# Kernel tuning notes

Measured on AMD Instinct MI355X. Metric: run time of the kernel, lower is better.

Reference implementation:

```python
import jax, jax.numpy as jnp
import numpy as np

NUM_GRAPHS = 100  # batch of graphs for pooling (dgl.max_nodes / WeightAndSum)


def _glorot(k, shape):
    lim = np.sqrt(6.0 / (shape[0] + shape[1])).astype(np.float32)
    return jax.random.uniform(k, shape, jnp.float32, -lim, lim)


def setup_inputs() -> dict:
    key = jax.random.key(0)
    ks = jax.random.split(key, 10)
    N, E, D, H = 100000, 1600000, 128, 128
    node_feats = jax.random.normal(ks[0], (N, D), dtype=jnp.float32)
    src = jax.random.randint(ks[1], (E,), 0, N, dtype=jnp.int32)
    dst = jax.random.randint(ks[2], (E,), 0, N, dtype=jnp.int32)
    graph_ids = jnp.sort(jax.random.randint(ks[3], (N,), 0, NUM_GRAPHS, dtype=jnp.int32))
    W1 = _glorot(ks[4], (D, H)); b1 = jnp.zeros((H,), jnp.float32)
    W2 = _glorot(ks[5], (H, H)); b2 = jnp.zeros((H,), jnp.float32)
    W3 = _glorot(ks[6], (H, H)); b3 = jnp.zeros((H,), jnp.float32)
    W_pool = _glorot(ks[7], (H, 1)); b_pool = jnp.zeros((1,), jnp.float32)
    return {"node_feats": node_feats, "src": src, "dst": dst, "graph_ids": graph_ids,
            "W1": W1, "b1": b1, "W2": W2, "b2": b2, "W3": W3, "b3": b3,
            "W_pool": W_pool, "b_pool": b_pool}


def _gcn_layer(h, W, b, src, dst, norm_src, norm_dst, N):
    # DGL GraphConv, norm='both': D_dst^{-1/2} (A^T (D_src^{-1/2} X W)) + b
    h = (h * norm_src[:, None]) @ W                      # [N, H]
    agg = jax.ops.segment_sum(h[src], dst, num_segments=N)  # gather + scatter-add
    return agg * norm_dst[:, None] + b


def reference(node_feats, src, dst, graph_ids, W1, b1, W2, b2, W3, b3, W_pool, b_pool):
    N = node_feats.shape[0]
    # dgl.add_self_loop (allow_zero_in_degree=False)
    loops = jnp.arange(N, dtype=src.dtype)
    src_sl = jnp.concatenate([src, loops])
    dst_sl = jnp.concatenate([dst, loops])
    ones = jnp.ones(src_sl.shape, jnp.float32)
    out_deg = jax.ops.segment_sum(ones, src_sl, num_segments=N)
    in_deg = jax.ops.segment_sum(ones, dst_sl, num_segments=N)
    norm_src = jax.lax.rsqrt(jnp.maximum(out_deg, 1.0))
    norm_dst = jax.lax.rsqrt(jnp.maximum(in_deg, 1.0))
    h = node_feats
    for W, b in ((W1, b1), (W2, b2), (W3, b3)):
        h = jax.nn.relu(_gcn_layer(h, W, b, src_sl, dst_sl, norm_src, norm_dst, N))
    # pooling_func: WeightAndSum (sigmoid-gated weighted sum per graph) + max_nodes
    w = jax.nn.sigmoid(h @ W_pool + b_pool)              # [N, 1]
    g_sum = jax.ops.segment_sum(h * w, graph_ids, num_segments=NUM_GRAPHS)
    g_max = jax.ops.segment_max(h, graph_ids, num_segments=NUM_GRAPHS)
    return jnp.concatenate([g_sum, g_max], axis=1)       # [G, 2H]
```

## Files before the change

kernel.cpp:

```cpp
#include <hip/hip_runtime.h>
#include <hip/hip_bf16.h>

#define DIM 128
#define CAP 64

typedef __attribute__((ext_vector_type(8))) short bf16x8;
typedef __attribute__((ext_vector_type(4))) float f32x4;
union U16 { uint4 u; bf16x8 b; };

__device__ __forceinline__ unsigned short f2bf(float f) {
    unsigned u = __float_as_uint(f);
    unsigned r = (u + 0x7fffu + ((u >> 16) & 1u)) >> 16;
    return (unsigned short)r;
}
__device__ __forceinline__ unsigned pack2bf(float a, float b) {
    return (unsigned)f2bf(a) | ((unsigned)f2bf(b) << 16);
}
__device__ __forceinline__ float2 unpack2bf(unsigned v) {
    float2 r;
    r.x = __uint_as_float(v << 16);
    r.y = __uint_as_float(v & 0xffff0000u);
    return r;
}
__device__ __forceinline__ void accum8(float* acc, uint4 v) {
    float2 f0 = unpack2bf(v.x), f1 = unpack2bf(v.y);
    float2 f2 = unpack2bf(v.z), f3 = unpack2bf(v.w);
    acc[0] += f0.x; acc[1] += f0.y; acc[2] += f1.x; acc[3] += f1.y;
    acc[4] += f2.x; acc[5] += f2.y; acc[6] += f3.x; acc[7] += f3.y;
}

__global__ __launch_bounds__(256) void k_build_gemm(const int* __restrict__ src,
                                                    const int* __restrict__ dst,
                                                    int* __restrict__ in_cnt,
                                                    int* __restrict__ out_cnt,
                                                    int* __restrict__ csr_pad, int E,
                                                    const float* __restrict__ x,
                                                    const float* __restrict__ W,
                                                    unsigned* __restrict__ xwb, int N,
                                                    int buildGrid, int mmGrid) {
    if (blockIdx.x & 1) {
        int bid = blockIdx.x >> 1;
        if (bid >= buildGrid) return;
        int e0 = (bid * 256 + threadIdx.x) * 4;
        int s[4], d[4], pos[4];
#pragma unroll
        for (int i = 0; i < 4; i++) {
            int e = e0 + i;
            if (e < E) { s[i] = src[e]; d[i] = dst[e]; }
        }
#pragma unroll
        for (int i = 0; i < 4; i++) {
            if (e0 + i < E) atomicAdd(&out_cnt[s[i]], 1);
        }
#pragma unroll
        for (int i = 0; i < 4; i++) {
            if (e0 + i < E) pos[i] = atomicAdd(&in_cnt[d[i]], 1);
        }
#pragma unroll
        for (int i = 0; i < 4; i++) {
            if (e0 + i < E && pos[i] < CAP) csr_pad[d[i] * CAP + pos[i]] = s[i];
        }
        return;
    }
    int bid = blockIdx.x >> 1;
    if (bid >= mmGrid) return;
    __shared__ float sW[32][128];
    __shared__ float sX[32][64];
    int t = threadIdx.x;
    int ty = t >> 4;
    int tx = t & 15;
    int nodeBase = bid * 64;

    float acc[4][8];
#pragma unroll
    for (int m = 0; m < 4; m++)
#pragma unroll
        for (int j = 0; j < 8; j++) acc[m][j] = 0.f;

    int ln = t & 63;
    int kb = (t >> 6) * 8;
    int nd = nodeBase + ln;

#pragma unroll 1
    for (int kc = 0; kc < DIM; kc += 32) {
#pragma unroll
        for (int i = 0; i < 4; i++) {
            int v = t + i * 256;
            int kk = v >> 5;
            int cc = (v & 31) * 4;
            *(float4*)&sW[kk][cc] = *(const float4*)&W[(kc + kk) * DIM + cc];
        }
        float4 a0, a1;
        if (nd < N) {
            a0 = *(const float4*)&x[nd * DIM + kc + kb];
            a1 = *(const float4*)&x[nd * DIM + kc + kb + 4];
        } else {
            a0 = make_float4(0, 0, 0, 0);
            a1 = make_float4(0, 0, 0, 0);
        }
        sX[kb + 0][ln] = a0.x;
        sX[kb + 1][ln] = a0.y;
        sX[kb + 2][ln] = a0.z;
        sX[kb + 3][ln] = a0.w;
        sX[kb + 4][ln] = a1.x;
        sX[kb + 5][ln] = a1.y;
        sX[kb + 6][ln] = a1.z;
        sX[kb + 7][ln] = a1.w;
        __syncthreads();

#pragma unroll
        for (int k = 0; k < 32; k++) {
            float4 xv = *(float4*)&sX[k][ty * 4];
            float4 wa = *(float4*)&sW[k][tx * 4];
            float4 wb = *(float4*)&sW[k][tx * 4 + 64];
            float xm[4] = {xv.x, xv.y, xv.z, xv.w};
#pragma unroll
            for (int m = 0; m < 4; m++) {
                acc[m][0] += xm[m] * wa.x;
                acc[m][1] += xm[m] * wa.y;
                acc[m][2] += xm[m] * wa.z;
                acc[m][3] += xm[m] * wa.w;
                acc[m][4] += xm[m] * wb.x;
                acc[m][5] += xm[m] * wb.y;
                acc[m][6] += xm[m] * wb.z;
                acc[m][7] += xm[m] * wb.w;
            }
        }
        __syncthreads();
    }

#pragma unroll
    for (int m = 0; m < 4; m++) {
        int n2 = nodeBase + ty * 4 + m;
        if (n2 < N) {
            uint2 q0, q1;
            q0.x = pack2bf(acc[m][0], acc[m][1]);
            q0.y = pack2bf(acc[m][2], acc[m][3]);
            q1.x = pack2bf(acc[m][4], acc[m][5]);
            q1.y = pack2bf(acc[m][6], acc[m][7]);
            *(uint2*)&xwb[n2 * 64 + tx * 2] = q0;
            *(uint2*)&xwb[n2 * 64 + 32 + tx * 2] = q1;
        }
    }
}

__global__ void k_finish(const int* __restrict__ in_cnt, const int* __restrict__ out_cnt,
                         float* __restrict__ nsrc, float* __restrict__ ndst, int N) {
    int i = blockIdx.x * blockDim.x + threadIdx.x;
    if (i < N) {
        nsrc[i] = rsqrtf((float)(out_cnt[i] + 1));
        ndst[i] = rsqrtf((float)(in_cnt[i] + 1));
    }
}

__global__ __launch_bounds__(256) void k_scale(unsigned* __restrict__ xwb,
                                               const float* __restrict__ nsrc, int total) {
    int i = blockIdx.x * blockDim.x + threadIdx.x;
    if (i < total) {
        float s = nsrc[i >> 6];
        float2 v = unpack2bf(xwb[i]);
        xwb[i] = pack2bf(v.x * s, v.y * s);
    }
}

__global__ __launch_bounds__(256) void k_xw_mfma(const unsigned* __restrict__ hb,
                                                 const float* __restrict__ nsrc,
                                                 const float* __restrict__ W,
                                                 unsigned* __restrict__ xwb, int N) {
    __shared__ unsigned wT[128 * 68];
    int t = threadIdx.x;
    {
        int n = t >> 1;
        int kp0 = (t & 1) * 32;
#pragma unroll
        for (int i = 0; i < 32; i++) {
            int kp = kp0 + i;
            wT[n * 68 + kp] = pack2bf(W[(2 * kp) * DIM + n], W[(2 * kp + 1) * DIM + n]);
        }
    }
    __syncthreads();
    int wave = t >> 6, lane = t & 63;
    int quad = lane >> 4, c = lane & 15;
    int m = blockIdx.x * 64 + wave * 16 + c;
    bool mv = m < N;
    f32x4 acc[8];
#pragma unroll
    for (int i = 0; i < 8; i++) acc[i] = (f32x4){0.f, 0.f, 0.f, 0.f};

#pragma unroll
    for (int ks = 0; ks < 4; ks++) {
        U16 av;
        if (mv) av.u = *(const uint4*)&hb[m * 64 + ks * 16 + quad * 4];
        else av.u = make_uint4(0, 0, 0, 0);
#pragma unroll
        for (int cb = 0; cb < 8; cb++) {
            U16 bv;
            bv.u = *(const uint4*)&wT[(cb * 16 + c) * 68 + ks * 16 + quad * 4];
            acc[cb] = __builtin_amdgcn_mfma_f32_16x16x32_bf16(av.b, bv.b, acc[cb], 0, 0, 0);
        }
    }
    int rowBase = blockIdx.x * 64 + wave * 16 + quad * 4;
#pragma unroll
    for (int r = 0; r < 4; r++) {
        int rowN = rowBase + r;
        float nrm = (rowN < N) ? nsrc[rowN] : 0.f;
#pragma unroll
        for (int cb = 0; cb < 8; cb++) {
            float v = acc[cb][r] * nrm;
            float vn = __shfl_xor(v, 1, 64);
            if (((c & 1) == 0) && rowN < N)
                xwb[rowN * 64 + cb * 8 + (c >> 1)] = pack2bf(v, vn);
        }
    }
}

template <bool GATED>
__device__ __forceinline__ void agg_body(const uint4* __restrict__ xwb4,
                                         const int* __restrict__ in_cnt,
                                         const int* __restrict__ csr_pad,
                                         const float* __restrict__ ndst,
                                         const float* __restrict__ bias,
                                         uint4* __restrict__ hb4,
                                         const float* __restrict__ Wp,
                                         const float* __restrict__ bp,
                                         float* __restrict__ wg, int N) {
    int gid = blockIdx.x * blockDim.x + threadIdx.x;
    int n = gid >> 6;
    int lane = gid & 63;
    if (n >= N) return;
    int quad = lane >> 4;
    int c = lane & 15;

    float acc[8];
#pragma unroll
    for (int i = 0; i < 8; i++) acc[i] = 0.f;

    if (quad == 0) {
        accum8(acc, xwb4[n * 16 + c]);
    }
    int deg = in_cnt[n];
    if (deg > CAP) deg = CAP;
    const int* row = &csr_pad[n * CAP];
    int p = 0;
    for (; p + 8 <= deg; p += 8) {
        int s0 = row[p + quad];
        int s1 = row[p + 4 + quad];
        uint4 v0 = xwb4[s0 * 16 + c];
        uint4 v1 = xwb4[s1 * 16 + c];
        accum8(acc, v0);
        accum8(acc, v1);
    }
    for (; p < deg; p += 4) {
        int pe = p + quad;
        int s = row[pe < deg ? pe : p];
        uint4 v = xwb4[s * 16 + c];
        if (pe < deg) accum8(acc, v);
    }
#pragma unroll
    for (int i = 0; i < 8; i++) {
        acc[i] += __shfl_xor(acc[i], 16, 64);
        acc[i] += __shfl_xor(acc[i], 32, 64);
    }
    float ndv = ndst[n];
    float4 b0 = ((const float4*)bias)[2 * c];
    float4 b1 = ((const float4*)bias)[2 * c + 1];
    float o[8];
    o[0] = fmaxf(acc[0] * ndv + b0.x, 0.f);
    o[1] = fmaxf(acc[1] * ndv + b0.y, 0.f);
    o[2] = fmaxf(acc[2] * ndv + b0.z, 0.f);
    o[3] = fmaxf(acc[3] * ndv + b0.w, 0.f);
    o[4] = fmaxf(acc[4] * ndv + b1.x, 0.f);
    o[5] = fmaxf(acc[5] * ndv + b1.y, 0.f);
    o[6] = fmaxf(acc[6] * ndv + b1.z, 0.f);
    o[7] = fmaxf(acc[7] * ndv + b1.w, 0.f);
    if (quad == 0) {
        uint4 w;
        w.x = pack2bf(o[0], o[1]);
        w.y = pack2bf(o[2], o[3]);
        w.z = pack2bf(o[4], o[5]);
        w.w = pack2bf(o[6], o[7]);
        hb4[n * 16 + c] = w;
    }
    if (GATED) {
        float s = 0.f;
        if (quad == 0) {
            float4 w0 = ((const float4*)Wp)[2 * c];
            float4 w1 = ((const float4*)Wp)[2 * c + 1];
            s = o[0] * w0.x + o[1] * w0.y + o[2] * w0.z + o[3] * w0.w +
                o[4] * w1.x + o[5] * w1.y + o[6] * w1.z + o[7] * w1.w;
        }
        s += __shfl_xor(s, 1, 64);
        s += __shfl_xor(s, 2, 64);
        s += __shfl_xor(s, 4, 64);
        s += __shfl_xor(s, 8, 64);
        if (lane == 0) wg[n] = 1.f / (1.f + expf(-(s + bp[0])));
    }
}

__global__ __launch_bounds__(256) void k_agg(const uint4* __restrict__ xwb4,
                                             const int* __restrict__ in_cnt,
                                             const int* __restrict__ csr_pad,
                                             const float* __restrict__ ndst,
                                             const float* __restrict__ bias,
                                             uint4* __restrict__ hb4, int N) {
    agg_body<false>(xwb4, in_cnt, csr_pad, ndst, bias, hb4, nullptr, nullptr, nullptr, N);
}

__global__ __launch_bounds__(256) void k_agg_gate(const uint4* __restrict__ xwb4,
                                                  const int* __restrict__ in_cnt,
                                                  const int* __restrict__ csr_pad,
                                                  const float* __restrict__ ndst,
                                                  const float* __restrict__ bias,
                                                  uint4* __restrict__ hb4,
                                                  const float* __restrict__ Wp,
                                                  const float* __restrict__ bp,
                                                  float* __restrict__ wg, int N) {
    agg_body<true>(xwb4, in_cnt, csr_pad, ndst, bias, hb4, Wp, bp, wg, N);
}

__device__ __forceinline__ int lower_bound(const int* a, int n, int key) {
    int lo = 0, hi = n;
    while (lo < hi) {
        int m = (lo + hi) >> 1;
        if (a[m] < key) lo = m + 1;
        else hi = m;
    }
    return lo;
}

__global__ __launch_bounds__(64) void k_pool(const unsigned* __restrict__ hb,
                                             const float* __restrict__ wg,
                                             const int* __restrict__ gids,
                                             float* __restrict__ out, int N) {
    int g = blockIdx.x >> 4;
    int part = blockIdx.x & 15;
    int t = threadIdx.x;
    int start = lower_bound(gids, N, g);
    int end = lower_bound(gids, N, g + 1);
    float2 sum = {0.f, 0.f}, mx = {0.f, 0.f};
    for (int n = start + part; n < end; n += 16) {
        float w = wg[n];
        float2 v = unpack2bf(hb[n * 64 + t]);
        sum.x += v.x * w;
        sum.y += v.y * w;
        mx.x = fmaxf(mx.x, v.x);
        mx.y = fmaxf(mx.y, v.y);
    }
    atomicAdd(&out[g * 256 + 2 * t], sum.x);
    atomicAdd(&out[g * 256 + 2 * t + 1], sum.y);
    atomicMax((int*)&out[g * 256 + 128 + 2 * t], __float_as_int(mx.x));
    atomicMax((int*)&out[g * 256 + 128 + 2 * t + 1], __float_as_int(mx.y));
}

extern "C" void kernel_launch(void* const* d_in, const int* in_sizes, int n_in,
                              void* d_out, int out_size, void* d_ws, size_t ws_size,
                              hipStream_t stream) {
    const float* node_feats = (const float*)d_in[0];
    const int* src = (const int*)d_in[1];
    const int* dst = (const int*)d_in[2];
    const int* gids = (const int*)d_in[3];
    const float* W1 = (const float*)d_in[4];
    const float* b1 = (const float*)d_in[5];
    const float* W2 = (const float*)d_in[6];
    const float* b2 = (const float*)d_in[7];
    const float* W3 = (const float*)d_in[8];
    const float* b3 = (const float*)d_in[9];
    const float* Wp = (const float*)d_in[10];
    const float* bp = (const float*)d_in[11];
    float* out = (float*)d_out;

    const int N = in_sizes[3];
    const int E = in_sizes[1];
    const int G = out_size / 256;

    char* ws = (char*)d_ws;
    size_t o = 0;
    int* in_cnt = (int*)(ws + o);        o += (size_t)N * 4;
    int* out_cnt = (int*)(ws + o);       o += (size_t)N * 4;
    size_t zero_bytes = o;
    float* nsrc = (float*)(ws + o);      o += (size_t)N * 4;
    float* ndst = (float*)(ws + o);      o += (size_t)N * 4;
    float* wg = (float*)(ws + o);        o += (size_t)N * 4;
    o = (o + 15) & ~15ull;
    int* csr_pad = (int*)(ws + o);       o += (size_t)N * CAP * 4;
    unsigned* xwb = (unsigned*)(ws + o); o += (size_t)N * 64 * 4;
    unsigned* hb = (unsigned*)(ws + o);  o += (size_t)N * 64 * 4;
    (void)ws_size;

    (void)hipMemsetAsync(d_ws, 0, zero_bytes, stream);
    (void)hipMemsetAsync(d_out, 0, (size_t)out_size * 4, stream);

    int buildGrid = ((E + 3) / 4 + 255) / 256;
    int mmGrid = (N + 63) / 64;
    int aggGrid = ((N * 64) + 255) / 256;
    int fusedGrid = 2 * (buildGrid > mmGrid ? buildGrid : mmGrid);

    k_build_gemm<<<fusedGrid, 256, 0, stream>>>(src, dst, in_cnt, out_cnt, csr_pad, E,
                                                node_feats, W1, xwb, N, buildGrid, mmGrid);
    k_finish<<<(N + 255) / 256, 256, 0, stream>>>(in_cnt, out_cnt, nsrc, ndst, N);
    k_scale<<<(N * 64 + 255) / 256, 256, 0, stream>>>(xwb, nsrc, N * 64);

    k_agg<<<aggGrid, 256, 0, stream>>>((const uint4*)xwb, in_cnt, csr_pad, ndst, b1,
                                       (uint4*)hb, N);
    k_xw_mfma<<<mmGrid, 256, 0, stream>>>(hb, nsrc, W2, xwb, N);
    k_agg<<<aggGrid, 256, 0, stream>>>((const uint4*)xwb, in_cnt, csr_pad, ndst, b2,
                                       (uint4*)hb, N);
    k_xw_mfma<<<mmGrid, 256, 0, stream>>>(hb, nsrc, W3, xwb, N);
    k_agg_gate<<<aggGrid, 256, 0, stream>>>((const uint4*)xwb, in_cnt, csr_pad, ndst, b3,
                                            (uint4*)hb, Wp, bp, wg, N);

    k_pool<<<G * 16, 64, 0, stream>>>(hb, wg, gids, out, N);
}
```

Measured before the change: 536.7 us.

## Fold degree normalization into aggregation and matmul, drop finish/scale kernels

Removes the separate norm-computing and source-scaling kernels. The degree norms are now computed inline with rsqrt from the degree counts. The first aggregation applies the source norm per gathered neighbor, and the later matmuls compute it from out_cnt directly. It also adds a 16-wide unrolled gather loop in aggregation to raise memory-level parallelism. In exchange, layer 1 does an extra out_cnt gather and rsqrt per edge.

```diff
diff --git a/kernel.cpp b/kernel.cpp
--- a/kernel.cpp
+++ b/kernel.cpp
@@ -22,11 +22,11 @@
     r.y = __uint_as_float(v & 0xffff0000u);
     return r;
 }
-__device__ __forceinline__ void accum8(float* acc, uint4 v) {
+__device__ __forceinline__ void accum8s(float* acc, uint4 v, float s) {
     float2 f0 = unpack2bf(v.x), f1 = unpack2bf(v.y);
     float2 f2 = unpack2bf(v.z), f3 = unpack2bf(v.w);
-    acc[0] += f0.x; acc[1] += f0.y; acc[2] += f1.x; acc[3] += f1.y;
-    acc[4] += f2.x; acc[5] += f2.y; acc[6] += f3.x; acc[7] += f3.y;
+    acc[0] += s * f0.x; acc[1] += s * f0.y; acc[2] += s * f1.x; acc[3] += s * f1.y;
+    acc[4] += s * f2.x; acc[5] += s * f2.y; acc[6] += s * f3.x; acc[7] += s * f3.y;
 }
 
 __global__ __launch_bounds__(256) void k_build_gemm(const int* __restrict__ src,
@@ -144,27 +144,8 @@
     }
 }
 
-__global__ void k_finish(const int* __restrict__ in_cnt, const int* __restrict__ out_cnt,
-                         float* __restrict__ nsrc, float* __restrict__ ndst, int N) {
-    int i = blockIdx.x * blockDim.x + threadIdx.x;
-    if (i < N) {
-        nsrc[i] = rsqrtf((float)(out_cnt[i] + 1));
-        ndst[i] = rsqrtf((float)(in_cnt[i] + 1));
-    }
-}
-
-__global__ __launch_bounds__(256) void k_scale(unsigned* __restrict__ xwb,
-                                               const float* __restrict__ nsrc, int total) {
-    int i = blockIdx.x * blockDim.x + threadIdx.x;
-    if (i < total) {
-        float s = nsrc[i >> 6];
-        float2 v = unpack2bf(xwb[i]);
-        xwb[i] = pack2bf(v.x * s, v.y * s);
-    }
-}
-
 __global__ __launch_bounds__(256) void k_xw_mfma(const unsigned* __restrict__ hb,
-                                                 const float* __restrict__ nsrc,
+                                                 const int* __restrict__ out_cnt,
                                                  const float* __restrict__ W,
                                                  unsigned* __restrict__ xwb, int N) {
     __shared__ unsigned wT[128 * 68];
@@ -203,7 +184,7 @@
 #pragma unroll
     for (int r = 0; r < 4; r++) {
         int rowN = rowBase + r;
-        float nrm = (rowN < N) ? nsrc[rowN] : 0.f;
+        float nrm = (rowN < N) ? rsqrtf((float)(out_cnt[rowN] + 1)) : 0.f;
 #pragma unroll
         for (int cb = 0; cb < 8; cb++) {
             float v = acc[cb][r] * nrm;
@@ -214,11 +195,11 @@
     }
 }
 
-template <bool GATED>
+template <bool GATED, bool SRCSCALE>
 __device__ __forceinline__ void agg_body(const uint4* __restrict__ xwb4,
                                          const int* __restrict__ in_cnt,
+                                         const int* __restrict__ out_cnt,
                                          const int* __restrict__ csr_pad,
-                                         const float* __restrict__ ndst,
                                          const float* __restrict__ bias,
                                          uint4* __restrict__ hb4,
                                          const float* __restrict__ Wp,
@@ -236,32 +217,62 @@
     for (int i = 0; i < 8; i++) acc[i] = 0.f;
 
     if (quad == 0) {
-        accum8(acc, xwb4[n * 16 + c]);
-    }
-    int deg = in_cnt[n];
-    if (deg > CAP) deg = CAP;
+        float sn = SRCSCALE ? rsqrtf((float)(out_cnt[n] + 1)) : 1.f;
+        accum8s(acc, xwb4[n * 16 + c], sn);
+    }
+    int deg_true = in_cnt[n];
+    int deg = deg_true > CAP ? CAP : deg_true;
     const int* row = &csr_pad[n * CAP];
     int p = 0;
+    for (; p + 16 <= deg; p += 16) {
+        int s0 = row[p + quad];
+        int s1 = row[p + 4 + quad];
+        int s2 = row[p + 8 + quad];
+        int s3 = row[p + 12 + quad];
+        uint4 v0 = xwb4[s0 * 16 + c];
+        uint4 v1 = xwb4[s1 * 16 + c];
+        uint4 v2 = xwb4[s2 * 16 + c];
+        uint4 v3 = xwb4[s3 * 16 + c];
+        float n0 = 1.f, n1 = 1.f, n2 = 1.f, n3 = 1.f;
+        if (SRCSCALE) {
+            int c0 = out_cnt[s0], c1 = out_cnt[s1], c2 = out_cnt[s2], c3 = out_cnt[s3];
+            n0 = rsqrtf((float)(c0 + 1));
+            n1 = rsqrtf((float)(c1 + 1));
+            n2 = rsqrtf((float)(c2 + 1));
+            n3 = rsqrtf((float)(c3 + 1));
+        }
+        accum8s(acc, v0, n0);
+        accum8s(acc, v1, n1);
+        accum8s(acc, v2, n2);
+        accum8s(acc, v3, n3);
+    }
     for (; p + 8 <= deg; p += 8) {
         int s0 = row[p + quad];
         int s1 = row[p + 4 + quad];
         uint4 v0 = xwb4[s0 * 16 + c];
         uint4 v1 = xwb4[s1 * 16 + c];
-        accum8(acc, v0);
-        accum8(acc, v1);
+        float n0 = 1.f, n1 = 1.f;
+        if (SRCSCALE) {
+            int c0 = out_cnt[s0], c1 = out_cnt[s1];
+            n0 = rsqrtf((float)(c0 + 1));
+            n1 = rsqrtf((float)(c1 + 1));
+        }
+        accum8s(acc, v0, n0);
+        accum8s(acc, v1, n1);
     }
     for (; p < deg; p += 4) {
         int pe = p + quad;
         int s = row[pe < deg ? pe : p];
         uint4 v = xwb4[s * 16 + c];
-        if (pe < deg) accum8(acc, v);
+        float ns = SRCSCALE ? rsqrtf((float)(out_cnt[s] + 1)) : 1.f;
+        if (pe < deg) accum8s(acc, v, ns);
     }
 #pragma unroll
     for (int i = 0; i < 8; i++) {
         acc[i] += __shfl_xor(acc[i], 16, 64);
         acc[i] += __shfl_xor(acc[i], 32, 64);
     }
-    float ndv = ndst[n];
+    float ndv = rsqrtf((float)(deg_true + 1));
     float4 b0 = ((const float4*)bias)[2 * c];
     float4 b1 = ((const float4*)bias)[2 * c + 1];
     float o[8];
@@ -297,25 +308,34 @@
     }
 }
 
+__global__ __launch_bounds__(256) void k_agg1(const uint4* __restrict__ xwb4,
+                                              const int* __restrict__ in_cnt,
+                                              const int* __restrict__ out_cnt,
+                                              const int* __restrict__ csr_pad,
+                                              const float* __restrict__ bias,
+                                              uint4* __restrict__ hb4, int N) {
+    agg_body<false, true>(xwb4, in_cnt, out_cnt, csr_pad, bias, hb4, nullptr, nullptr,
+                          nullptr, N);
+}
+
 __global__ __launch_bounds__(256) void k_agg(const uint4* __restrict__ xwb4,
                                              const int* __restrict__ in_cnt,
                                              const int* __restrict__ csr_pad,
-                                             const float* __restrict__ ndst,
                                              const float* __restrict__ bias,
                                              uint4* __restrict__ hb4, int N) {
-    agg_body<false>(xwb4, in_cnt, csr_pad, ndst, bias, hb4, nullptr, nullptr, nullptr, N);
+    agg_body<false, false>(xwb4, in_cnt, nullptr, csr_pad, bias, hb4, nullptr, nullptr,
+                           nullptr, N);
 }
 
 __global__ __launch_bounds__(256) void k_agg_gate(const uint4* __restrict__ xwb4,
                                                   const int* __restrict__ in_cnt,
                                                   const int* __restrict__ csr_pad,
-                                                  const float* __restrict__ ndst,
                                                   const float* __restrict__ bias,
                                                   uint4* __restrict__ hb4,
                                                   const float* __restrict__ Wp,
                                                   const float* __restrict__ bp,
                                                   float* __restrict__ wg, int N) {
-    agg_body<true>(xwb4, in_cnt, csr_pad, ndst, bias, hb4, Wp, bp, wg, N);
+    agg_body<true, false>(xwb4, in_cnt, nullptr, csr_pad, bias, hb4, Wp, bp, wg, N);
 }
 
 __device__ __forceinline__ int lower_bound(const int* a, int n, int key) {
@@ -378,8 +398,6 @@
     int* in_cnt = (int*)(ws + o);        o += (size_t)N * 4;
     int* out_cnt = (int*)(ws + o);       o += (size_t)N * 4;
     size_t zero_bytes = o;
-    float* nsrc = (float*)(ws + o);      o += (size_t)N * 4;
-    float* ndst = (float*)(ws + o);      o += (size_t)N * 4;
     float* wg = (float*)(ws + o);        o += (size_t)N * 4;
     o = (o + 15) & ~15ull;
     int* csr_pad = (int*)(ws + o);       o += (size_t)N * CAP * 4;
@@ -397,16 +415,14 @@
 
     k_build_gemm<<<fusedGrid, 256, 0, stream>>>(src, dst, in_cnt, out_cnt, csr_pad, E,
                                                 node_feats, W1, xwb, N, buildGrid, mmGrid);
-    k_finish<<<(N + 255) / 256, 256, 0, stream>>>(in_cnt, out_cnt, nsrc, ndst, N);
-    k_scale<<<(N * 64 + 255) / 256, 256, 0, stream>>>(xwb, nsrc, N * 64);
-
-    k_agg<<<aggGrid, 256, 0, stream>>>((const uint4*)xwb, in_cnt, csr_pad, ndst, b1,
+
+    k_agg1<<<aggGrid, 256, 0, stream>>>((const uint4*)xwb, in_cnt, out_cnt, csr_pad, b1,
+                                        (uint4*)hb, N);
+    k_xw_mfma<<<mmGrid, 256, 0, stream>>>(hb, out_cnt, W2, xwb, N);
+    k_agg<<<aggGrid, 256, 0, stream>>>((const uint4*)xwb, in_cnt, csr_pad, b2,
                                        (uint4*)hb, N);
-    k_xw_mfma<<<mmGrid, 256, 0, stream>>>(hb, nsrc, W2, xwb, N);
-    k_agg<<<aggGrid, 256, 0, stream>>>((const uint4*)xwb, in_cnt, csr_pad, ndst, b2,
-                                       (uint4*)hb, N);
-    k_xw_mfma<<<mmGrid, 256, 0, stream>>>(hb, nsrc, W3, xwb, N);
-    k_agg_gate<<<aggGrid, 256, 0, stream>>>((const uint4*)xwb, in_cnt, csr_pad, ndst, b3,
+    k_xw_mfma<<<mmGrid, 256, 0, stream>>>(hb, out_cnt, W3, xwb, N);
+    k_agg_gate<<<aggGrid, 256, 0, stream>>>((const uint4*)xwb, in_cnt, csr_pad, b3,
                                             (uint4*)hb, Wp, bp, wg, N);
 
     k_pool<<<G * 16, 64, 0, stream>>>(hb, wg, gids, out, N);
```

New measurement: 508.9 us. 5.2% less time.
